# Optimization experiments

Hardware: AMD Instinct MI355X
Metric: run time of the kernel (lower is better)

Reference implementation:

```python
import jax, jax.numpy as jnp
import numpy as np

N, D = 65536, 512

def setup_inputs() -> dict:
    key = jax.random.key(0)
    k1, k2, k3, k4, k5 = jax.random.split(key, 5)
    lim = 1.0 / np.sqrt(D)
    inputs = jax.random.normal(k1, (N, D), dtype=jnp.float32)
    key_w = jax.random.uniform(k2, (1, D), minval=-lim, maxval=lim, dtype=jnp.float32)
    key_b = jax.random.uniform(k3, (1,), minval=-lim, maxval=lim, dtype=jnp.float32)
    value_w = jax.random.uniform(k4, (D, D), minval=-lim, maxval=lim, dtype=jnp.float32)
    value_b = jax.random.uniform(k5, (D,), minval=-lim, maxval=lim, dtype=jnp.float32)
    return {"inputs": inputs, "key_w": key_w, "key_b": key_b,
            "value_w": value_w, "value_b": value_b}

def reference(inputs, key_w, key_b, value_w, value_b):
    # key: [N,1], value: [N,D] (torch Linear: x @ W.T + b)
    k = inputs @ key_w.T + key_b            # [N,1]
    v = inputs @ value_w.T + value_b        # [N,D]
    # Reassociate (v @ inputs.T) @ k == v @ (inputs.T @ k): avoids O(N^2) intermediate
    s = inputs.T @ k                        # [D,1]
    x = v @ s                               # [N,1]
    return jax.nn.softmax(x, axis=0)        # softmax over nodes (dim=0)
```

## Files before the change

### kernel.cpp

```cpp
#include <hip/hip_runtime.h>
#include <float.h>

#define NROWS 65536
#define DDIM  512
#define NBLK_A 512
#define NBLK_C 1024

#define WS_T   4096
#define WS_MP  4608
#define WS_LP  5632

__global__ __launch_bounds__(256, 2) void kA(const float* __restrict__ in,
                                             const float* __restrict__ key_w,
                                             const float* __restrict__ key_b,
                                             float* __restrict__ s8) {
    const int tid  = threadIdx.x;
    const int lane = tid & 63;
    const int wv   = tid >> 6;
    const int q    = lane >> 5;
    const int u    = lane & 31;
    const int gw   = blockIdx.x * 4 + wv;

    const float4* kw4 = (const float4*)key_w;
    float4 kw[4];
    #pragma unroll
    for (int j = 0; j < 4; ++j) kw[j] = kw4[u + j * 32];
    const float kb = key_b[0];

    float4 acc[4];
    #pragma unroll
    for (int j = 0; j < 4; ++j) acc[j] = make_float4(0.f, 0.f, 0.f, 0.f);

    #pragma unroll
    for (int g = 0; g < 2; ++g) {
        const int rowbase = (gw + g * 2048) * 16;
        #pragma unroll
        for (int it = 0; it < 8; ++it) {
            const int row = rowbase + it * 2 + q;
            const float4* r4 = (const float4*)(in + (size_t)row * DDIM);
            float4 v[4];
            #pragma unroll
            for (int j = 0; j < 4; ++j) v[j] = r4[u + j * 32];
            float p = 0.f;
            #pragma unroll
            for (int j = 0; j < 4; ++j)
                p += v[j].x * kw[j].x + v[j].y * kw[j].y
                   + v[j].z * kw[j].z + v[j].w * kw[j].w;
            #pragma unroll
            for (int o = 1; o < 32; o <<= 1) p += __shfl_xor(p, o, 64);
            const float k = p + kb;
            #pragma unroll
            for (int j = 0; j < 4; ++j) {
                acc[j].x += k * v[j].x; acc[j].y += k * v[j].y;
                acc[j].z += k * v[j].z; acc[j].w += k * v[j].w;
            }
        }
    }

    #pragma unroll
    for (int j = 0; j < 4; ++j) {
        acc[j].x += __shfl_xor(acc[j].x, 32, 64);
        acc[j].y += __shfl_xor(acc[j].y, 32, 64);
        acc[j].z += __shfl_xor(acc[j].z, 32, 64);
        acc[j].w += __shfl_xor(acc[j].w, 32, 64);
    }

    __shared__ float sb[4][DDIM];
    if (q == 0) {
        #pragma unroll
        for (int j = 0; j < 4; ++j) {
            const int c = 4 * (u + j * 32);
            sb[wv][c]     = acc[j].x;
            sb[wv][c + 1] = acc[j].y;
            sb[wv][c + 2] = acc[j].z;
            sb[wv][c + 3] = acc[j].w;
        }
    }
    __syncthreads();

    float* dst = s8 + (size_t)(blockIdx.x & 7) * DDIM;
    atomicAdd(&dst[tid],       sb[0][tid]     + sb[1][tid]     + sb[2][tid]     + sb[3][tid]);
    atomicAdd(&dst[tid + 256], sb[0][tid+256] + sb[1][tid+256] + sb[2][tid+256] + sb[3][tid+256]);
}

__global__ __launch_bounds__(512) void kB(const float* __restrict__ vw,
                                          const float* __restrict__ s8,
                                          float* __restrict__ t) {
    const int j = threadIdx.x;
    float acc = 0.f;
    #pragma unroll
    for (int ii = 0; ii < 8; ++ii) {
        const int i = blockIdx.x * 8 + ii;
        float si = 0.f;
        #pragma unroll
        for (int c = 0; c < 8; ++c) si += s8[c * 512 + i];
        acc += vw[(size_t)i * 512 + j] * si;
    }
    atomicAdd(&t[j], acc);
}

__global__ __launch_bounds__(256, 4) void kC(const float* __restrict__ in,
                                             const float* __restrict__ t,
                                             float* __restrict__ x,
                                             float* __restrict__ mpart,
                                             float* __restrict__ lpart) {
    const int tid  = threadIdx.x;
    const int lane = tid & 63;
    const int wv   = tid >> 6;
    const int q    = lane >> 5;
    const int u    = lane & 31;
    const int gw   = blockIdx.x * 4 + wv;

    const float4* t4 = (const float4*)t;
    float4 tt[4];
    #pragma unroll
    for (int j = 0; j < 4; ++j) tt[j] = t4[u + j * 32];

    float m = -FLT_MAX, l = 0.f;
    const int rowbase = gw * 16;
    #pragma unroll
    for (int it = 0; it < 8; ++it) {
        const int row = rowbase + it * 2 + q;
        const float4* r4 = (const float4*)(in + (size_t)row * DDIM);
        float4 v[4];
        #pragma unroll
        for (int j = 0; j < 4; ++j) v[j] = r4[u + j * 32];
        float p = 0.f;
        #pragma unroll
        for (int j = 0; j < 4; ++j)
            p += v[j].x * tt[j].x + v[j].y * tt[j].y
               + v[j].z * tt[j].z + v[j].w * tt[j].w;
        #pragma unroll
        for (int o = 1; o < 32; o <<= 1) p += __shfl_xor(p, o, 64);
        if (u == 0) x[row] = p;
        const float mn = fmaxf(m, p);
        l = l * __expf(m - mn) + __expf(p - mn);
        m = mn;
    }

    {
        const float mo = __shfl_xor(m, 32, 64);
        const float lo = __shfl_xor(l, 32, 64);
        const float mn = fmaxf(m, mo);
        l = l * __expf(m - mn) + lo * __expf(mo - mn);
        m = mn;
    }
    __shared__ float ms[4], ls[4];
    if (lane == 0) { ms[wv] = m; ls[wv] = l; }
    __syncthreads();
    if (tid == 0) {
        m = ms[0]; l = ls[0];
        #pragma unroll
        for (int w = 1; w < 4; ++w) {
            const float mn = fmaxf(m, ms[w]);
            l = l * __expf(m - mn) + ls[w] * __expf(ms[w] - mn);
            m = mn;
        }
        mpart[blockIdx.x] = m;
        lpart[blockIdx.x] = l;
    }
}

__global__ __launch_bounds__(256) void kE(float* __restrict__ x,
                                          const float* __restrict__ mpart,
                                          const float* __restrict__ lpart) {
    const int tid  = threadIdx.x;
    const int lane = tid & 63;
    const int wv   = tid >> 6;

    float m = -FLT_MAX, l = 0.f;
    #pragma unroll
    for (int j = 0; j < 4; ++j) {
        const float mp = mpart[tid * 4 + j];
        const float lp = lpart[tid * 4 + j];
        const float mn = fmaxf(m, mp);
        l = l * __expf(m - mn) + lp * __expf(mp - mn);
        m = mn;
    }
    #pragma unroll
    for (int o = 1; o < 64; o <<= 1) {
        const float mo = __shfl_xor(m, o, 64);
        const float lo = __shfl_xor(l, o, 64);
        const float mn = fmaxf(m, mo);
        l = l * __expf(m - mn) + lo * __expf(mo - mn);
        m = mn;
    }
    __shared__ float ms[4], ls[4];
    __shared__ float Ms, Ls;
    if (lane == 0) { ms[wv] = m; ls[wv] = l; }
    __syncthreads();
    if (tid == 0) {
        m = ms[0]; l = ls[0];
        #pragma unroll
        for (int w = 1; w < 4; ++w) {
            const float mn = fmaxf(m, ms[w]);
            l = l * __expf(m - mn) + ls[w] * __expf(ms[w] - mn);
            m = mn;
        }
        Ms = m; Ls = l;
    }
    __syncthreads();

    float4* x4 = (float4*)x;
    const int i = blockIdx.x * 256 + tid;
    float4 v = x4[i];
    const float inv = 1.0f / Ls;
    v.x = __expf(v.x - Ms) * inv;
    v.y = __expf(v.y - Ms) * inv;
    v.z = __expf(v.z - Ms) * inv;
    v.w = __expf(v.w - Ms) * inv;
    x4[i] = v;
}

extern "C" void kernel_launch(void* const* d_in, const int* in_sizes, int n_in,
                              void* d_out, int out_size, void* d_ws, size_t ws_size,
                              hipStream_t stream) {
    const float* in    = (const float*)d_in[0];
    const float* key_w = (const float*)d_in[1];
    const float* key_b = (const float*)d_in[2];
    const float* vw    = (const float*)d_in[3];

    float* ws    = (float*)d_ws;
    float* s8    = ws;
    float* t     = ws + WS_T;
    float* mpart = ws + WS_MP;
    float* lpart = ws + WS_LP;
    float* out   = (float*)d_out;

    kA<<<NBLK_A, 256, 0, stream>>>(in, key_w, key_b, s8);
    kB<<<64, 512, 0, stream>>>(vw, s8, t);
    kC<<<NBLK_C, 256, 0, stream>>>(in, t, out, mpart, lpart);
    kE<<<64, 256, 0, stream>>>(out, mpart, lpart);
}
```

Measured before the change: 220.6 us.

## Restage key-weighted row sum through swizzled shared-memory tiles

The first pass, which computes inputs^T @ k, now loads 16-row tiles into shared memory with an XOR swizzle. Each 16-thread group computes one row's key dot product, and then every thread accumulates two output columns across the tile from shared memory. This replaces the per-wave register accumulators and cross-wave shuffle and shared reduction. It also doubles the block count to 1024 and raises the occupancy hint to 4. The cost is two barriers per tile and a 32KB shared tile per block, which may limit occupancy.

```diff
diff --git a/kernel.cpp b/kernel.cpp
--- a/kernel.cpp
+++ b/kernel.cpp
@@ -3,84 +3,72 @@
 
 #define NROWS 65536
 #define DDIM  512
-#define NBLK_A 512
+#define NBLK_A 1024
 #define NBLK_C 1024
 
 #define WS_T   4096
 #define WS_MP  4608
 #define WS_LP  5632
 
-__global__ __launch_bounds__(256, 2) void kA(const float* __restrict__ in,
-                                             const float* __restrict__ key_w,
-                                             const float* __restrict__ key_b,
-                                             float* __restrict__ s8) {
+__global__ __launch_bounds__(256, 4) void kAF(const float* __restrict__ in,
+                                              const float* __restrict__ key_w,
+                                              const float* __restrict__ key_b,
+                                              float* __restrict__ s8) {
     const int tid  = threadIdx.x;
-    const int lane = tid & 63;
-    const int wv   = tid >> 6;
-    const int q    = lane >> 5;
-    const int u    = lane & 31;
-    const int gw   = blockIdx.x * 4 + wv;
-
+    const int row  = tid >> 4;
+    const int part = tid & 15;
+    const int blk  = blockIdx.x;
+
+    __shared__ float4 tile4[16 * 128];
+    __shared__ float  k_tile[16];
+    float* tileF = (float*)tile4;
+
+    const float4* in4 = (const float4*)in;
     const float4* kw4 = (const float4*)key_w;
-    float4 kw[4];
-    #pragma unroll
-    for (int j = 0; j < 4; ++j) kw[j] = kw4[u + j * 32];
-    const float kb = key_b[0];
-
-    float4 acc[4];
-    #pragma unroll
-    for (int j = 0; j < 4; ++j) acc[j] = make_float4(0.f, 0.f, 0.f, 0.f);
-
-    #pragma unroll
-    for (int g = 0; g < 2; ++g) {
-        const int rowbase = (gw + g * 2048) * 16;
-        #pragma unroll
-        for (int it = 0; it < 8; ++it) {
-            const int row = rowbase + it * 2 + q;
-            const float4* r4 = (const float4*)(in + (size_t)row * DDIM);
-            float4 v[4];
-            #pragma unroll
-            for (int j = 0; j < 4; ++j) v[j] = r4[u + j * 32];
-            float p = 0.f;
-            #pragma unroll
-            for (int j = 0; j < 4; ++j)
-                p += v[j].x * kw[j].x + v[j].y * kw[j].y
-                   + v[j].z * kw[j].z + v[j].w * kw[j].w;
-            #pragma unroll
-            for (int o = 1; o < 32; o <<= 1) p += __shfl_xor(p, o, 64);
-            const float k = p + kb;
-            #pragma unroll
-            for (int j = 0; j < 4; ++j) {
-                acc[j].x += k * v[j].x; acc[j].y += k * v[j].y;
-                acc[j].z += k * v[j].z; acc[j].w += k * v[j].w;
-            }
-        }
-    }
-
-    #pragma unroll
-    for (int j = 0; j < 4; ++j) {
-        acc[j].x += __shfl_xor(acc[j].x, 32, 64);
-        acc[j].y += __shfl_xor(acc[j].y, 32, 64);
-        acc[j].z += __shfl_xor(acc[j].z, 32, 64);
-        acc[j].w += __shfl_xor(acc[j].w, 32, 64);
-    }
-
-    __shared__ float sb[4][DDIM];
-    if (q == 0) {
-        #pragma unroll
-        for (int j = 0; j < 4; ++j) {
-            const int c = 4 * (u + j * 32);
-            sb[wv][c]     = acc[j].x;
-            sb[wv][c + 1] = acc[j].y;
-            sb[wv][c + 2] = acc[j].z;
-            sb[wv][c + 3] = acc[j].w;
-        }
-    }
-    __syncthreads();
-
-    float* dst = s8 + (size_t)(blockIdx.x & 7) * DDIM;
-    atomicAdd(&dst[tid],       sb[0][tid]     + sb[1][tid]     + sb[2][tid]     + sb[3][tid]);
-    atomicAdd(&dst[tid + 256], sb[0][tid+256] + sb[1][tid+256] + sb[2][tid+256] + sb[3][tid+256]);
+    const float   kb  = key_b[0];
+
+    float4 kwv[8];
+    #pragma unroll
+    for (int j = 0; j < 8; ++j) kwv[j] = kw4[part * 8 + j];
+
+    const int c4s = tid >> 1;
+    const int swr = (c4s & 0x78) | ((c4s & 7) ^ ((c4s >> 3) & 7));
+    const int rdo = swr * 4 + (tid & 1) * 2;
+
+    float s0 = 0.f, s1 = 0.f;
+
+    for (int tilei = 0; tilei < 4; ++tilei) {
+        const int base = blk * 64 + tilei * 16;
+
+        float p = 0.f;
+        const size_t gbase = (size_t)(base + row) * 128;
+        #pragma unroll
+        for (int j = 0; j < 8; ++j) {
+            const int col4 = part * 8 + j;
+            float4 g = in4[gbase + col4];
+            p += g.x * kwv[j].x + g.y * kwv[j].y
+               + g.z * kwv[j].z + g.w * kwv[j].w;
+            const int sw = part * 8 + (j ^ (part & 7));
+            tile4[row * 128 + sw] = g;
+        }
+        #pragma unroll
+        for (int o = 1; o < 16; o <<= 1) p += __shfl_xor(p, o, 64);
+        if (part == 0) k_tile[row] = p + kb;
+        __syncthreads();
+
+        #pragma unroll
+        for (int r = 0; r < 16; ++r) {
+            const float kr = k_tile[r];
+            const float2 v = *(const float2*)&tileF[r * 512 + rdo];
+            s0 += kr * v.x;
+            s1 += kr * v.y;
+        }
+        __syncthreads();
+    }
+
+    float* dst = s8 + (size_t)(blk & 7) * DDIM;
+    atomicAdd(&dst[2 * tid],     s0);
+    atomicAdd(&dst[2 * tid + 1], s1);
 }
 
 __global__ __launch_bounds__(512) void kB(const float* __restrict__ vw,
@@ -227,7 +215,7 @@
     float* lpart = ws + WS_LP;
     float* out   = (float*)d_out;
 
-    kA<<<NBLK_A, 256, 0, stream>>>(in, key_w, key_b, s8);
+    kAF<<<NBLK_A, 256, 0, stream>>>(in, key_w, key_b, s8);
     kB<<<64, 512, 0, stream>>>(vw, s8, t);
     kC<<<NBLK_C, 256, 0, stream>>>(in, t, out, mpart, lpart);
     kE<<<64, 256, 0, stream>>>(out, mpart, lpart);
```

New measurement: 255.0 us. 1.16x slower.
